# Performance work log

Hardware: AMD Instinct MI355X
Metric: run time of the kernel (lower is better)

The kernel has to match this reference:

```python
import jax, jax.numpy as jnp
import numpy as np

NUM_NODE = 100000
DEG = 16
E = NUM_NODE * DEG
IN_C = 128
HID_C = 128
NUM_REL = 8


def setup_inputs() -> dict:
    key = jax.random.key(0)
    k1, k2, k3, k4, k5, k6 = jax.random.split(key, 6)
    x = jax.random.normal(k1, (NUM_NODE, IN_C), dtype=jnp.float32)
    # glorot-style init for relation weights [num_rel, in, hid]
    scale = jnp.sqrt(6.0 / (IN_C + HID_C)).astype(jnp.float32)
    rel_weight = jax.random.uniform(k2, (NUM_REL, IN_C, HID_C), dtype=jnp.float32, minval=-1.0, maxval=1.0) * scale
    # uniform-degree CSR so every node has deg >= 1 (avoids div-by-zero, matches module assumption)
    ptr = jnp.arange(NUM_NODE + 1, dtype=jnp.int64) * DEG
    idx = jax.random.randint(k3, (E,), 0, NUM_NODE, dtype=jnp.int64)
    edge_types = jax.random.randint(k4, (E,), 0, NUM_REL, dtype=jnp.int64)
    # about 1/3 of nodes have cached history (value != -1)
    history_map = jax.random.randint(k5, (NUM_NODE,), -1, 2, dtype=jnp.int64)
    history_buffer = jax.random.normal(k6, (NUM_NODE, HID_C), dtype=jnp.float32)
    return {
        'x': x,
        'rel_weight': rel_weight,
        'ptr': ptr,
        'idx': idx,
        'edge_types': edge_types,
        'history_map': history_map,
        'history_buffer': history_buffer,
        'history_size': 1,
        'num_node': NUM_NODE,
    }


def reference(x, rel_weight, ptr, idx, edge_types, history_map, history_buffer, history_size, num_node):
    E_ = idx.shape[0]
    num_rel = rel_weight.shape[0]
    hid = rel_weight.shape[2]
    xg = x[idx]                                   # [E, in] gather of source features
    # relation-grouped transform: small static loop over relations, masked accumulate
    msgs = jnp.zeros((E_, hid), dtype=x.dtype)
    for r in range(num_rel):
        msgs = msgs + jnp.where((edge_types == r)[:, None], xg @ rel_weight[r], jnp.zeros((), x.dtype))
    deg = ptr[1:] - ptr[:-1]                      # [num_node]
    seg = jnp.repeat(jnp.arange(num_node), deg, total_repeat_length=E_)  # dst id per edge
    out = jax.ops.segment_sum(msgs, seg, num_segments=num_node)          # scatter-sum
    out = out / deg[:, None].astype(out.dtype)    # degree normalization
    if history_size > 0:                          # static python int
        out = jnp.where((history_map != -1)[:, None], history_buffer, out)
    return (out, out)
```

## Files before the change

### kernel.cpp

```cpp
#include <hip/hip_runtime.h>
#include <stdint.h>

#define IN_C   128
#define HID_C  128
#define NREL   8
#define K_TOTAL (NREL * IN_C)
#define TILE_M  16
#define SRB     1032

typedef float  f32x4  __attribute__((ext_vector_type(4)));
typedef __bf16 bf16x8 __attribute__((ext_vector_type(8)));
typedef short  s16x8  __attribute__((ext_vector_type(8)));
typedef unsigned short u16;

__device__ __forceinline__ unsigned short f2bf(float f) {
    unsigned int u = __float_as_uint(f);
    u += 0x7fffu + ((u >> 16) & 1u);
    return (unsigned short)(u >> 16);
}

__global__ void zero_count_kernel(unsigned int* count) { *count = 0u; }

__global__ __launch_bounds__(256) void prep_kernel(
        const float* __restrict__ x, const float* __restrict__ W,
        const int* __restrict__ hmap, const float* __restrict__ hbuf,
        unsigned short* __restrict__ xh, unsigned short* __restrict__ Wt,
        int* __restrict__ list, unsigned int* __restrict__ count,
        float* __restrict__ out, int NN, int WE, int use_xh) {
    int gid = blockIdx.x * blockDim.x + threadIdx.x;

    {
        bool active = (gid < NN) && (hmap[gid] == -1);
        unsigned long long mask = __ballot(active);
        if (mask) {
            int lane   = threadIdx.x & 63;
            int leader = __ffsll((unsigned long long)mask) - 1;
            unsigned base = 0;
            if (lane == leader) base = atomicAdd(count, (unsigned)__popcll(mask));
            base = __shfl(base, leader, 64);
            if (active) {
                int off = __popcll(mask & ((1ull << lane) - 1ull));
                list[base + off] = gid;
            }
        }
    }

    int n = gid >> 5;
    int q = gid & 31;
    if (n < NN) {
        if (use_xh) {
            f32x4 xv = ((const f32x4*)x)[(size_t)n * 32 + q];
            ushort4 pk;
            pk.x = f2bf(xv[0]); pk.y = f2bf(xv[1]);
            pk.z = f2bf(xv[2]); pk.w = f2bf(xv[3]);
            ((ushort4*)xh)[(size_t)n * 32 + q] = pk;
        }
        if (hmap[n] != -1) {
            f32x4 v = ((const f32x4*)hbuf)[(size_t)n * 32 + q];
            f32x4* o = (f32x4*)out;
            o[(size_t)n * 32 + q] = v;
            o[(size_t)NN * 32 + (size_t)n * 32 + q] = v;
        }
    }

    if (gid < WE) {
        int r   = gid >> 14;
        int rem = gid & 16383;
        int k   = rem >> 7;
        int c   = rem & 127;
        Wt[(size_t)c * K_TOTAL + r * IN_C + k] = f2bf(W[gid]);
    }
}

template<int XBF>
__global__ __launch_bounds__(256, 4) void gemm_kernel_t(
        const float* __restrict__ x,
        const unsigned short* __restrict__ xh,
        const int* __restrict__ ptr,
        const int* __restrict__ idx,
        const int* __restrict__ ety,
        const unsigned short* __restrict__ Wt,
        const int* __restrict__ list,
        const unsigned int* __restrict__ count,
        float* __restrict__ out, int NN) {
    __shared__ u16      S[TILE_M * SRB];
    __shared__ unsigned meta[TILE_M * 16];
    __shared__ int      nids[TILE_M];
    __shared__ int      degs[TILE_M];
    __shared__ float    invdeg[TILE_M];

    unsigned int cnt = *count;
    int rowbase = blockIdx.x * TILE_M;
    if (rowbase >= (int)cnt) return;

    int t = threadIdx.x;
    if (t < TILE_M) {
        int row = rowbase + t;
        int nid = -1, d = 0; float idg = 0.f;
        if (row < (int)cnt) {
            nid = list[row];
            int e0 = ptr[nid], e1 = ptr[nid + 1];
            d = e1 - e0;
            idg = (d > 0) ? 1.0f / (float)d : 0.f;
        }
        nids[t] = nid; degs[t] = d; invdeg[t] = idg;
    }
    __syncthreads();

    int n = t >> 4;
    int c = t & 15;
    int nid = nids[n];
    int deg = degs[n];
    int e0  = (nid >= 0) ? ptr[nid] : 0;

    int maxdeg = 0;
    #pragma unroll
    for (int i = 0; i < TILE_M; ++i) maxdeg = max(maxdeg, degs[i]);

    f32x4 alo[NREL], ahi[NREL];
    #pragma unroll
    for (int r = 0; r < NREL; ++r) { alo[r] = f32x4{0,0,0,0}; ahi[r] = f32x4{0,0,0,0}; }

    const char* xcb = XBF ? ((const char*)xh + c * 16)
                          : ((const char*)x  + c * 32);

    auto accum_bf = [&](uint4 v, unsigned m) {
        int r_ = (int)(m >> 27);
        f32x4 lo_, hi_;
        lo_[0] = __uint_as_float(v.x << 16);
        lo_[1] = __uint_as_float(v.x & 0xFFFF0000u);
        lo_[2] = __uint_as_float(v.y << 16);
        lo_[3] = __uint_as_float(v.y & 0xFFFF0000u);
        hi_[0] = __uint_as_float(v.z << 16);
        hi_[1] = __uint_as_float(v.z & 0xFFFF0000u);
        hi_[2] = __uint_as_float(v.w << 16);
        hi_[3] = __uint_as_float(v.w & 0xFFFF0000u);
        #pragma unroll
        for (int rr = 0; rr < NREL; ++rr) {
            float mk = (r_ == rr) ? 1.0f : 0.0f;
            alo[rr] += lo_ * mk;
            ahi[rr] += hi_ * mk;
        }
    };
    auto accum_f32 = [&](f32x4 lo_, f32x4 hi_, unsigned m) {
        int r_ = (int)(m >> 27);
        #pragma unroll
        for (int rr = 0; rr < NREL; ++rr) {
            float mk = (r_ == rr) ? 1.0f : 0.0f;
            alo[rr] += lo_ * mk;
            ahi[rr] += hi_ * mk;
        }
    };

    for (int jb = 0; jb < maxdeg; jb += 16) {
        {
            int j = jb + c;
            unsigned m = 31u << 27;
            if (nid >= 0 && j < deg) {
                int e = e0 + j;
                m = ((unsigned)idx[e]) | (((unsigned)ety[e]) << 27);
            }
            meta[t] = m;
        }
        __syncthreads();

        unsigned mm[16];
        {
            uint4 q0 = *(const uint4*)(meta + (n << 4) + 0);
            uint4 q1 = *(const uint4*)(meta + (n << 4) + 4);
            uint4 q2 = *(const uint4*)(meta + (n << 4) + 8);
            uint4 q3 = *(const uint4*)(meta + (n << 4) + 12);
            mm[0]=q0.x;  mm[1]=q0.y;  mm[2]=q0.z;  mm[3]=q0.w;
            mm[4]=q1.x;  mm[5]=q1.y;  mm[6]=q1.z;  mm[7]=q1.w;
            mm[8]=q2.x;  mm[9]=q2.y;  mm[10]=q2.z; mm[11]=q2.w;
            mm[12]=q3.x; mm[13]=q3.y; mm[14]=q3.z; mm[15]=q3.w;
        }

        if (XBF) {
            uint4 cur[4];
            #pragma unroll
            for (int u = 0; u < 4; ++u)
                cur[u] = *(const uint4*)(xcb + ((size_t)(mm[u] & 0x07FFFFFFu) << 8));
            #pragma unroll
            for (int b = 0; b < 4; ++b) {
                uint4 nxt[4];
                if (b < 3) {
                    #pragma unroll
                    for (int u = 0; u < 4; ++u)
                        nxt[u] = *(const uint4*)(xcb + ((size_t)(mm[(b+1)*4+u] & 0x07FFFFFFu) << 8));
                }
                #pragma unroll
                for (int u = 0; u < 4; ++u) accum_bf(cur[u], mm[b*4+u]);
                if (b < 3) {
                    #pragma unroll
                    for (int u = 0; u < 4; ++u) cur[u] = nxt[u];
                }
            }
        } else {
            f32x4 clo[4], chi[4];
            #pragma unroll
            for (int u = 0; u < 4; ++u) {
                const f32x4* p = (const f32x4*)(xcb + ((size_t)(mm[u] & 0x07FFFFFFu) << 9));
                clo[u] = p[0]; chi[u] = p[1];
            }
            #pragma unroll
            for (int b = 0; b < 4; ++b) {
                f32x4 nlo[4], nhi[4];
                if (b < 3) {
                    #pragma unroll
                    for (int u = 0; u < 4; ++u) {
                        const f32x4* p = (const f32x4*)(xcb + ((size_t)(mm[(b+1)*4+u] & 0x07FFFFFFu) << 9));
                        nlo[u] = p[0]; nhi[u] = p[1];
                    }
                }
                #pragma unroll
                for (int u = 0; u < 4; ++u) accum_f32(clo[u], chi[u], mm[b*4+u]);
                if (b < 3) {
                    #pragma unroll
                    for (int u = 0; u < 4; ++u) { clo[u] = nlo[u]; chi[u] = nhi[u]; }
                }
            }
        }
        __syncthreads();
    }

    {
        u16* srow = S + n * SRB + c * 8;
        #pragma unroll
        for (int rr = 0; rr < NREL; ++rr) {
            s16x8 pk;
            pk[0] = (short)f2bf(alo[rr][0]); pk[1] = (short)f2bf(alo[rr][1]);
            pk[2] = (short)f2bf(alo[rr][2]); pk[3] = (short)f2bf(alo[rr][3]);
            pk[4] = (short)f2bf(ahi[rr][0]); pk[5] = (short)f2bf(ahi[rr][1]);
            pk[6] = (short)f2bf(ahi[rr][2]); pk[7] = (short)f2bf(ahi[rr][3]);
            *(s16x8*)(srow + rr * IN_C) = pk;
        }
    }
    __syncthreads();

    int wave = t >> 6, lane = t & 63;
    int quad = lane >> 4, l16 = lane & 15;
    int chbase = wave * 32;
    const u16* arow  = S + l16 * SRB + quad * 8;
    const u16* bbase = Wt + (size_t)(chbase + l16) * K_TOTAL + quad * 8;

    f32x4 acc0 = {0.f,0.f,0.f,0.f};
    f32x4 acc1 = {0.f,0.f,0.f,0.f};
    #pragma unroll 8
    for (int ks = 0; ks < K_TOTAL; ks += 32) {
        s16x8 a  = *(const s16x8*)(arow + ks);
        s16x8 b0 = *(const s16x8*)(bbase + ks);
        s16x8 b1 = *(const s16x8*)(bbase + ks + 16 * K_TOTAL);
        union { s16x8 s; bf16x8 b; } ua, ub0, ub1;
        ua.s = a; ub0.s = b0; ub1.s = b1;
        acc0 = __builtin_amdgcn_mfma_f32_16x16x32_bf16(ua.b, ub0.b, acc0, 0, 0, 0);
        acc1 = __builtin_amdgcn_mfma_f32_16x16x32_bf16(ua.b, ub1.b, acc1, 0, 0, 0);
    }

    size_t half = (size_t)NN * HID_C;
    #pragma unroll
    for (int v = 0; v < 4; ++v) {
        int rowl = quad * 4 + v;
        int onid = nids[rowl];
        if (onid < 0) continue;
        float s = invdeg[rowl];
        float v0 = acc0[v] * s;
        float v1 = acc1[v] * s;
        size_t o0 = (size_t)onid * HID_C + chbase + l16;
        out[o0]             = v0;
        out[o0 + 16]        = v1;
        out[o0 + half]      = v0;
        out[o0 + 16 + half] = v1;
    }
}

extern "C" void kernel_launch(void* const* d_in, const int* in_sizes, int n_in,
                              void* d_out, int out_size, void* d_ws, size_t ws_size,
                              hipStream_t stream) {
    const float* x    = (const float*)d_in[0];
    const float* W    = (const float*)d_in[1];
    const int*   ptr  = (const int*)d_in[2];
    const int*   idx  = (const int*)d_in[3];
    const int*   ety  = (const int*)d_in[4];
    const int*   hmap = (const int*)d_in[5];
    const float* hbuf = (const float*)d_in[6];
    int NN = in_sizes[5];
    int WE = in_sizes[1];
    float* out = (float*)d_out;

    unsigned int* count = (unsigned int*)d_ws;
    int* list = (int*)((char*)d_ws + 256);
    size_t wt_off = 256 + (((size_t)NN * 4 + 4095) / 4096) * 4096;
    unsigned short* Wt = (unsigned short*)((char*)d_ws + wt_off);
    size_t xh_off = ((wt_off + (size_t)K_TOTAL * HID_C * 2 + 4095) / 4096) * 4096;
    unsigned short* xh = (unsigned short*)((char*)d_ws + xh_off);
    size_t need = xh_off + (size_t)NN * IN_C * 2;
    int use_xh = (ws_size >= need) ? 1 : 0;

    zero_count_kernel<<<1, 1, 0, stream>>>(count);

    long long tot = (long long)NN * 32;
    if (tot < (long long)WE) tot = WE;
    prep_kernel<<<(int)((tot + 255) / 256), 256, 0, stream>>>(
        x, W, hmap, hbuf, xh, Wt, list, count, out, NN, WE, use_xh);

    int gblocks = (NN + TILE_M - 1) / TILE_M;
    if (use_xh) {
        gemm_kernel_t<1><<<gblocks, 256, 0, stream>>>(
            x, xh, ptr, idx, ety, Wt, list, count, out, NN);
    } else {
        gemm_kernel_t<0><<<gblocks, 256, 0, stream>>>(
            x, xh, ptr, idx, ety, Wt, list, count, out, NN);
    }
}
```

Baseline: 300.7 us.

## Make gemm kernel persistent and overlap next tile's gather with current MFMA

Converts the gather+GEMM kernel into a persistent grid of fixed size that loops over tiles with a grid stride. It prefetches the next tile's metadata and first half of the neighbor gathers before running the MFMA GEMM for the previous tile, so gather latency can be hidden behind matrix work. Edge metadata is broadcast with wave shuffles instead of going through shared memory. Occupancy hint drops from 4 to 3 blocks per CU to fit the extra live registers, and the fixed grid may underfill or imbalance the GPU.

```diff
diff --git a/kernel.cpp b/kernel.cpp
--- a/kernel.cpp
+++ b/kernel.cpp
@@ -7,6 +7,7 @@
 #define K_TOTAL (NREL * IN_C)
 #define TILE_M  16
 #define SRB     1032
+#define GEMM_GRID 768
 
 typedef float  f32x4  __attribute__((ext_vector_type(4)));
 typedef __bf16 bf16x8 __attribute__((ext_vector_type(8)));
@@ -73,7 +74,7 @@
 }
 
 template<int XBF>
-__global__ __launch_bounds__(256, 4) void gemm_kernel_t(
+__global__ __launch_bounds__(256, 3) void gemm_kernel_t(
         const float* __restrict__ x,
         const unsigned short* __restrict__ xh,
         const int* __restrict__ ptr,
@@ -83,46 +84,47 @@
         const int* __restrict__ list,
         const unsigned int* __restrict__ count,
         float* __restrict__ out, int NN) {
-    __shared__ u16      S[TILE_M * SRB];
-    __shared__ unsigned meta[TILE_M * 16];
-    __shared__ int      nids[TILE_M];
-    __shared__ int      degs[TILE_M];
-    __shared__ float    invdeg[TILE_M];
+    constexpr int LW = XBF ? 1 : 2;
+    __shared__ u16   S[TILE_M * SRB];
+    __shared__ int   nids_l[TILE_M];
+    __shared__ float invd_l[TILE_M];
 
     unsigned int cnt = *count;
-    int rowbase = blockIdx.x * TILE_M;
-    if (rowbase >= (int)cnt) return;
+    int ntiles = (int)((cnt + TILE_M - 1) / TILE_M);
+    int tile_p = blockIdx.x;
+    if (tile_p >= ntiles) return;
 
     int t = threadIdx.x;
-    if (t < TILE_M) {
-        int row = rowbase + t;
-        int nid = -1, d = 0; float idg = 0.f;
-        if (row < (int)cnt) {
-            nid = list[row];
-            int e0 = ptr[nid], e1 = ptr[nid + 1];
-            d = e1 - e0;
-            idg = (d > 0) ? 1.0f / (float)d : 0.f;
-        }
-        nids[t] = nid; degs[t] = d; invdeg[t] = idg;
-    }
-    __syncthreads();
-
     int n = t >> 4;
     int c = t & 15;
-    int nid = nids[n];
-    int deg = degs[n];
-    int e0  = (nid >= 0) ? ptr[nid] : 0;
-
-    int maxdeg = 0;
-    #pragma unroll
-    for (int i = 0; i < TILE_M; ++i) maxdeg = max(maxdeg, degs[i]);
-
-    f32x4 alo[NREL], ahi[NREL];
-    #pragma unroll
-    for (int r = 0; r < NREL; ++r) { alo[r] = f32x4{0,0,0,0}; ahi[r] = f32x4{0,0,0,0}; }
-
+    int lane = t & 63;
+    int wave = t >> 6;
+    int quad = lane >> 4, l16 = lane & 15;
+    int chbase = wave * 32;
+    const u16* arow  = S + l16 * SRB + quad * 8;
+    const u16* bbase = Wt + (size_t)(chbase + l16) * K_TOTAL + quad * 8;
     const char* xcb = XBF ? ((const char*)xh + c * 16)
                           : ((const char*)x  + c * 32);
+    int stride = (int)gridDim.x;
+
+    auto stage1 = [&](int T, int& nid_, int& e0_, int& deg_, unsigned& m_) {
+        nid_ = -1; e0_ = 0; deg_ = 0; m_ = 31u << 27;
+        if (T < ntiles) {
+            int row = T * TILE_M + n;
+            if (row < (int)cnt) {
+                int nd = list[row];
+                nid_ = nd;
+                int a = ptr[nd], b2 = ptr[nd + 1];
+                e0_ = a; deg_ = b2 - a;
+                if (c < deg_) {
+                    int e = a + c;
+                    m_ = ((unsigned)idx[e]) | (((unsigned)ety[e]) << 27);
+                }
+            }
+        }
+    };
+
+    f32x4 alo[NREL], ahi[NREL];
 
     auto accum_bf = [&](uint4 v, unsigned m) {
         int r_ = (int)(m >> 27);
@@ -142,8 +144,13 @@
             ahi[rr] += hi_ * mk;
         }
     };
-    auto accum_f32 = [&](f32x4 lo_, f32x4 hi_, unsigned m) {
+    auto accum_f32 = [&](uint4 a, uint4 b, unsigned m) {
         int r_ = (int)(m >> 27);
+        f32x4 lo_, hi_;
+        lo_[0] = __uint_as_float(a.x); lo_[1] = __uint_as_float(a.y);
+        lo_[2] = __uint_as_float(a.z); lo_[3] = __uint_as_float(a.w);
+        hi_[0] = __uint_as_float(b.x); hi_[1] = __uint_as_float(b.y);
+        hi_[2] = __uint_as_float(b.z); hi_[3] = __uint_as_float(b.w);
         #pragma unroll
         for (int rr = 0; rr < NREL; ++rr) {
             float mk = (r_ == rr) ? 1.0f : 0.0f;
@@ -152,125 +159,131 @@
         }
     };
 
-    for (int jb = 0; jb < maxdeg; jb += 16) {
+    int nidP, e0P, degP; unsigned mP;
+    stage1(tile_p, nidP, e0P, degP, mP);
+
+    bool haveC = false;
+
+    for (;;) {
+        bool haveP = (tile_p < ntiles);
+        unsigned mm[16];
+        uint4 gA[8 * LW];
+        int nidN = -1, e0N = 0, degN = 0; unsigned mN = 31u << 27;
+
+        if (haveP) {
+            stage1(tile_p + stride, nidN, e0N, degN, mN);
+            #pragma unroll
+            for (int j = 0; j < 16; ++j)
+                mm[j] = __shfl(mP, (lane & 48) | j, 64);
+            #pragma unroll
+            for (int u = 0; u < 8; ++u) {
+                const char* p = xcb + ((size_t)(mm[u] & 0x07FFFFFFu) << (XBF ? 8 : 9));
+                gA[u * LW] = *(const uint4*)p;
+                if (!XBF) gA[u * LW + 1] = *(const uint4*)(p + 16);
+            }
+        }
+        __builtin_amdgcn_sched_barrier(0);
+
+        if (haveC) {
+            f32x4 acc0 = {0.f,0.f,0.f,0.f};
+            f32x4 acc1 = {0.f,0.f,0.f,0.f};
+            #pragma unroll 8
+            for (int ks = 0; ks < K_TOTAL; ks += 32) {
+                s16x8 a  = *(const s16x8*)(arow + ks);
+                s16x8 b0 = *(const s16x8*)(bbase + ks);
+                s16x8 b1 = *(const s16x8*)(bbase + ks + 16 * K_TOTAL);
+                union { s16x8 s; bf16x8 b; } ua, ub0, ub1;
+                ua.s = a; ub0.s = b0; ub1.s = b1;
+                acc0 = __builtin_amdgcn_mfma_f32_16x16x32_bf16(ua.b, ub0.b, acc0, 0, 0, 0);
+                acc1 = __builtin_amdgcn_mfma_f32_16x16x32_bf16(ua.b, ub1.b, acc1, 0, 0, 0);
+            }
+            size_t half = (size_t)NN * HID_C;
+            #pragma unroll
+            for (int v = 0; v < 4; ++v) {
+                int rowl = quad * 4 + v;
+                int onid = nids_l[rowl];
+                if (onid < 0) continue;
+                float s = invd_l[rowl];
+                float v0 = acc0[v] * s;
+                float v1 = acc1[v] * s;
+                size_t o0 = (size_t)onid * HID_C + chbase + l16;
+                out[o0]             = v0;
+                out[o0 + 16]        = v1;
+                out[o0 + half]      = v0;
+                out[o0 + 16 + half] = v1;
+            }
+        }
+        __syncthreads();
+        if (!haveP) break;
+
         {
-            int j = jb + c;
-            unsigned m = 31u << 27;
-            if (nid >= 0 && j < deg) {
-                int e = e0 + j;
-                m = ((unsigned)idx[e]) | (((unsigned)ety[e]) << 27);
-            }
-            meta[t] = m;
-        }
-        __syncthreads();
-
-        unsigned mm[16];
-        {
-            uint4 q0 = *(const uint4*)(meta + (n << 4) + 0);
-            uint4 q1 = *(const uint4*)(meta + (n << 4) + 4);
-            uint4 q2 = *(const uint4*)(meta + (n << 4) + 8);
-            uint4 q3 = *(const uint4*)(meta + (n << 4) + 12);
-            mm[0]=q0.x;  mm[1]=q0.y;  mm[2]=q0.z;  mm[3]=q0.w;
-            mm[4]=q1.x;  mm[5]=q1.y;  mm[6]=q1.z;  mm[7]=q1.w;
-            mm[8]=q2.x;  mm[9]=q2.y;  mm[10]=q2.z; mm[11]=q2.w;
-            mm[12]=q3.x; mm[13]=q3.y; mm[14]=q3.z; mm[15]=q3.w;
-        }
-
-        if (XBF) {
-            uint4 cur[4];
-            #pragma unroll
-            for (int u = 0; u < 4; ++u)
-                cur[u] = *(const uint4*)(xcb + ((size_t)(mm[u] & 0x07FFFFFFu) << 8));
-            #pragma unroll
-            for (int b = 0; b < 4; ++b) {
-                uint4 nxt[4];
-                if (b < 3) {
-                    #pragma unroll
-                    for (int u = 0; u < 4; ++u)
-                        nxt[u] = *(const uint4*)(xcb + ((size_t)(mm[(b+1)*4+u] & 0x07FFFFFFu) << 8));
+            #pragma unroll
+            for (int r = 0; r < NREL; ++r) {
+                alo[r] = f32x4{0,0,0,0}; ahi[r] = f32x4{0,0,0,0};
+            }
+            uint4 gB[8 * LW];
+            #pragma unroll
+            for (int u = 0; u < 8; ++u) {
+                const char* p = xcb + ((size_t)(mm[8 + u] & 0x07FFFFFFu) << (XBF ? 8 : 9));
+                gB[u * LW] = *(const uint4*)p;
+                if (!XBF) gB[u * LW + 1] = *(const uint4*)(p + 16);
+            }
+            #pragma unroll
+            for (int u = 0; u < 8; ++u) {
+                if (XBF) accum_bf(gA[u], mm[u]);
+                else     accum_f32(gA[u * 2], gA[u * 2 + 1], mm[u]);
+            }
+            #pragma unroll
+            for (int u = 0; u < 8; ++u) {
+                if (XBF) accum_bf(gB[u], mm[8 + u]);
+                else     accum_f32(gB[u * 2], gB[u * 2 + 1], mm[8 + u]);
+            }
+
+            int md = degP;
+            #pragma unroll
+            for (int off = 1; off <= 32; off <<= 1)
+                md = max(md, __shfl_xor(md, off, 64));
+            for (int jb = 16; jb < md; jb += 16) {
+                unsigned m2 = 31u << 27;
+                if (nidP >= 0 && jb + c < degP) {
+                    int e = e0P + jb + c;
+                    m2 = ((unsigned)idx[e]) | (((unsigned)ety[e]) << 27);
                 }
                 #pragma unroll
-                for (int u = 0; u < 4; ++u) accum_bf(cur[u], mm[b*4+u]);
-                if (b < 3) {
-                    #pragma unroll
-                    for (int u = 0; u < 4; ++u) cur[u] = nxt[u];
-                }
-            }
-        } else {
-            f32x4 clo[4], chi[4];
-            #pragma unroll
-            for (int u = 0; u < 4; ++u) {
-                const f32x4* p = (const f32x4*)(xcb + ((size_t)(mm[u] & 0x07FFFFFFu) << 9));
-                clo[u] = p[0]; chi[u] = p[1];
-            }
-            #pragma unroll
-            for (int b = 0; b < 4; ++b) {
-                f32x4 nlo[4], nhi[4];
-                if (b < 3) {
-                    #pragma unroll
-                    for (int u = 0; u < 4; ++u) {
-                        const f32x4* p = (const f32x4*)(xcb + ((size_t)(mm[(b+1)*4+u] & 0x07FFFFFFu) << 9));
-                        nlo[u] = p[0]; nhi[u] = p[1];
+                for (int j = 0; j < 16; ++j) {
+                    unsigned mx = __shfl(m2, (lane & 48) | j, 64);
+                    const char* p = xcb + ((size_t)(mx & 0x07FFFFFFu) << (XBF ? 8 : 9));
+                    if (XBF) {
+                        uint4 g = *(const uint4*)p;
+                        accum_bf(g, mx);
+                    } else {
+                        uint4 g0 = *(const uint4*)p;
+                        uint4 g1 = *(const uint4*)(p + 16);
+                        accum_f32(g0, g1, mx);
                     }
                 }
-                #pragma unroll
-                for (int u = 0; u < 4; ++u) accum_f32(clo[u], chi[u], mm[b*4+u]);
-                if (b < 3) {
-                    #pragma unroll
-                    for (int u = 0; u < 4; ++u) { clo[u] = nlo[u]; chi[u] = nhi[u]; }
-                }
+            }
+
+            u16* srow = S + n * SRB + c * 8;
+            #pragma unroll
+            for (int rr = 0; rr < NREL; ++rr) {
+                s16x8 pk;
+                pk[0] = (short)f2bf(alo[rr][0]); pk[1] = (short)f2bf(alo[rr][1]);
+                pk[2] = (short)f2bf(alo[rr][2]); pk[3] = (short)f2bf(alo[rr][3]);
+                pk[4] = (short)f2bf(ahi[rr][0]); pk[5] = (short)f2bf(ahi[rr][1]);
+                pk[6] = (short)f2bf(ahi[rr][2]); pk[7] = (short)f2bf(ahi[rr][3]);
+                *(s16x8*)(srow + rr * IN_C) = pk;
+            }
+            if (c == 0) {
+                nids_l[n] = nidP;
+                invd_l[n] = (degP > 0) ? 1.0f / (float)degP : 0.f;
             }
         }
         __syncthreads();
-    }
-
-    {
-        u16* srow = S + n * SRB + c * 8;
-        #pragma unroll
-        for (int rr = 0; rr < NREL; ++rr) {
-            s16x8 pk;
-            pk[0] = (short)f2bf(alo[rr][0]); pk[1] = (short)f2bf(alo[rr][1]);
-            pk[2] = (short)f2bf(alo[rr][2]); pk[3] = (short)f2bf(alo[rr][3]);
-            pk[4] = (short)f2bf(ahi[rr][0]); pk[5] = (short)f2bf(ahi[rr][1]);
-            pk[6] = (short)f2bf(ahi[rr][2]); pk[7] = (short)f2bf(ahi[rr][3]);
-            *(s16x8*)(srow + rr * IN_C) = pk;
-        }
-    }
-    __syncthreads();
-
-    int wave = t >> 6, lane = t & 63;
-    int quad = lane >> 4, l16 = lane & 15;
-    int chbase = wave * 32;
-    const u16* arow  = S + l16 * SRB + quad * 8;
-    const u16* bbase = Wt + (size_t)(chbase + l16) * K_TOTAL + quad * 8;
-
-    f32x4 acc0 = {0.f,0.f,0.f,0.f};
-    f32x4 acc1 = {0.f,0.f,0.f,0.f};
-    #pragma unroll 8
-    for (int ks = 0; ks < K_TOTAL; ks += 32) {
-        s16x8 a  = *(const s16x8*)(arow + ks);
-        s16x8 b0 = *(const s16x8*)(bbase + ks);
-        s16x8 b1 = *(const s16x8*)(bbase + ks + 16 * K_TOTAL);
-        union { s16x8 s; bf16x8 b; } ua, ub0, ub1;
-        ua.s = a; ub0.s = b0; ub1.s = b1;
-        acc0 = __builtin_amdgcn_mfma_f32_16x16x32_bf16(ua.b, ub0.b, acc0, 0, 0, 0);
-        acc1 = __builtin_amdgcn_mfma_f32_16x16x32_bf16(ua.b, ub1.b, acc1, 0, 0, 0);
-    }
-
-    size_t half = (size_t)NN * HID_C;
-    #pragma unroll
-    for (int v = 0; v < 4; ++v) {
-        int rowl = quad * 4 + v;
-        int onid = nids[rowl];
-        if (onid < 0) continue;
-        float s = invdeg[rowl];
-        float v0 = acc0[v] * s;
-        float v1 = acc1[v] * s;
-        size_t o0 = (size_t)onid * HID_C + chbase + l16;
-        out[o0]             = v0;
-        out[o0 + 16]        = v1;
-        out[o0 + half]      = v0;
-        out[o0 + 16 + half] = v1;
+
+        haveC = true;
+        tile_p += stride;
+        nidP = nidN; e0P = e0N; degP = degN; mP = mN;
     }
 }
 
@@ -304,12 +317,11 @@
     prep_kernel<<<(int)((tot + 255) / 256), 256, 0, stream>>>(
         x, W, hmap, hbuf, xh, Wt, list, count, out, NN, WE, use_xh);
 
-    int gblocks = (NN + TILE_M - 1) / TILE_M;
     if (use_xh) {
-        gemm_kernel_t<1><<<gblocks, 256, 0, stream>>>(
+        gemm_kernel_t<1><<<GEMM_GRID, 256, 0, stream>>>(
             x, xh, ptr, idx, ety, Wt, list, count, out, NN);
     } else {
-        gemm_kernel_t<0><<<gblocks, 256, 0, stream>>>(
+        gemm_kernel_t<0><<<GEMM_GRID, 256, 0, stream>>>(
             x, xh, ptr, idx, ety, Wt, list, count, out, NN);
     }
 }
```

Measured after the change: 457.3 us. 52.1% more time.
